# Performance work log

Measured on AMD Instinct MI355X. Metric: run time of the kernel, lower is better.

The kernel has to match this reference:

```python
import jax, jax.numpy as jnp
import numpy as np


def setup_inputs() -> dict:
    key = jax.random.key(0)
    kq, kk, kv = jax.random.split(key, 3)
    B, S, D = 4, 4096, 64
    q = jax.random.normal(kq, (B, S, D), dtype=jnp.float32)
    k = jax.random.normal(kk, (B, S, D), dtype=jnp.float32)
    v = jax.random.normal(kv, (B, S, D), dtype=jnp.float32)
    return {"q": q, "k": k, "v": v}


def reference(q, k, v):
    # Faithful math of the original blocked loop:
    #   output_i += exp(Q_i @ K_j^T) @ V_j, summed over all column blocks j
    # which is exactly unnormalized exponential attention:
    #   out = exp(Q K^T) V  (no 1/sqrt(d) scaling, no softmax normalization,
    #   no max-subtraction -- matching the source module's math).
    scores = jnp.einsum("bqd,bkd->bqk", q, k)  # [B, Sq, Sk]
    return jnp.einsum("bqk,bkd->bqd", jnp.exp(scores), v)  # [B, Sq, D]
```

## Files before the change

kernel.cpp:

```cpp
#include <hip/hip_runtime.h>
#include <hip/hip_bf16.h>


typedef short    s16x4 __attribute__((ext_vector_type(4)));
typedef short    s16x8 __attribute__((ext_vector_type(8)));
typedef _Float16 h16x8 __attribute__((ext_vector_type(8)));
typedef float    fx4   __attribute__((ext_vector_type(4)));
typedef float    fx16  __attribute__((ext_vector_type(16)));

constexpr int S = 4096, D = 64, BQ = 64, BN = 64;
constexpr int KH = 4;
constexpr int NT = S / BN / KH;

__device__ __forceinline__ unsigned short f2bf(float x) {
    unsigned u = __float_as_uint(x);
    u = (u + 0x7FFFu + ((u >> 16) & 1u)) >> 16;
    return (unsigned short)u;
}
__device__ __forceinline__ float bf2f(unsigned short h) {
    return __uint_as_float(((unsigned)h) << 16);
}
__device__ __forceinline__ unsigned short f2h(float x) {
    union { _Float16 h; unsigned short s; } u;
    u.h = (_Float16)x;
    return u.s;
}
__device__ __forceinline__ unsigned pack_bf16(float lo, float hi) {
    __hip_bfloat162 r = __float22bfloat162_rn(make_float2(lo, hi));
    union { __hip_bfloat162 b; unsigned u; } c;
    c.b = r;
    return c.u;
}

__global__ __launch_bounds__(256, 4) void attn_fused(
    const float* __restrict__ q, const float* __restrict__ k,
    const float* __restrict__ v, float* __restrict__ partial)
{
    __shared__ unsigned short Ks[64 * 72];
    __shared__ unsigned short Vt[64 * 72];
    __shared__ float red[4096];

    const int tid = threadIdx.x, lane = tid & 63, w = tid >> 6;
    const int h = lane >> 5, m5 = lane & 31;
    const int mt = w & 1, kkh = w >> 1;
    const int b = blockIdx.y, q0 = blockIdx.x * BQ, kh = blockIdx.z;

    const float* kbase = k + ((size_t)b * S + (size_t)kh * NT * BN) * D;
    const float* vbase = v + ((size_t)b * S + (size_t)kh * NT * BN) * D;

    h16x8 qf[4];
    {
        const float* qrow = q + ((size_t)b * S + q0 + mt * 32 + m5) * D + h * 8;
        #pragma unroll
        for (int ks = 0; ks < 4; ++ks) {
            float4 a = *(const float4*)(qrow + ks * 16);
            float4 c = *(const float4*)(qrow + ks * 16 + 4);
            qf[ks] = (h16x8){(_Float16)a.x, (_Float16)a.y, (_Float16)a.z, (_Float16)a.w,
                             (_Float16)c.x, (_Float16)c.y, (_Float16)c.z, (_Float16)c.w};
        }
    }

    const int krow0 = tid >> 4;
    const int kc4   = (tid & 15) << 2;
    const int vd    = tid & 63;
    const int vg    = w;

    float4 kraw[4];
    float  vraw[16];

    auto load_raw = [&](int t) {
        const float* kt = kbase + (size_t)t * BN * D;
        const float* vt = vbase + (size_t)t * BN * D;
        #pragma unroll
        for (int i = 0; i < 4; ++i)
            kraw[i] = *(const float4*)(kt + (i * 16 + krow0) * D + kc4);
        #pragma unroll
        for (int j = 0; j < 16; ++j)
            vraw[j] = vt[(vg * 16 + j) * D + vd];
    };

    auto cvt_store = [&]() {
        #pragma unroll
        for (int i = 0; i < 4; ++i) {
            s16x4 o = {(short)f2h(kraw[i].x), (short)f2h(kraw[i].y),
                       (short)f2h(kraw[i].z), (short)f2h(kraw[i].w)};
            *(s16x4*)&Ks[(i * 16 + krow0) * 72 + kc4] = o;
        }
        union { unsigned u[4]; s16x8 v; } p0, p1;
        #pragma unroll
        for (int jj = 0; jj < 4; ++jj) {
            p0.u[jj] = pack_bf16(vraw[2 * jj],     vraw[2 * jj + 1]);
            p1.u[jj] = pack_bf16(vraw[8 + 2 * jj], vraw[9 + 2 * jj]);
        }
        *(s16x8*)&Vt[vd * 72 + vg * 16]     = p0.v;
        *(s16x8*)&Vt[vd * 72 + vg * 16 + 8] = p1.v;
    };

    fx16 oacc[2] = {};

    load_raw(0);
    for (int t = 0; t < NT; ++t) {
        cvt_store();
        __syncthreads();
        if (t + 1 < NT) load_raw(t + 1);

        fx16 sa = {};
        #pragma unroll
        for (int ks = 0; ks < 4; ++ks) {
            h16x8 a = *(const h16x8*)&Ks[(kkh * 32 + m5) * 72 + ks * 16 + h * 8];
            sa = __builtin_amdgcn_mfma_f32_32x32x16_f16(a, qf[ks], sa, 0, 0, 0);
        }

        unsigned p01[8];
        #pragma unroll
        for (int rp = 0; rp < 8; ++rp)
            p01[rp] = pack_bf16(__expf(sa[2 * rp]), __expf(sa[2 * rp + 1]));

        union frag { unsigned u[4]; s16x8 v; };
        frag A[2];
#if __has_builtin(__builtin_amdgcn_permlane32_swap)
        typedef unsigned uix2 __attribute__((ext_vector_type(2)));
        uix2 r0 = __builtin_amdgcn_permlane32_swap(p01[0], p01[2], false, false);
        uix2 r1 = __builtin_amdgcn_permlane32_swap(p01[1], p01[3], false, false);
        A[0].u[0] = r0.x; A[0].u[1] = r1.x; A[0].u[2] = r0.y; A[0].u[3] = r1.y;
        uix2 r2 = __builtin_amdgcn_permlane32_swap(p01[4], p01[6], false, false);
        uix2 r3 = __builtin_amdgcn_permlane32_swap(p01[5], p01[7], false, false);
        A[1].u[0] = r2.x; A[1].u[1] = r3.x; A[1].u[2] = r2.y; A[1].u[3] = r3.y;
#else
        unsigned sw[8];
        #pragma unroll
        for (int rp = 0; rp < 8; ++rp)
            sw[rp] = (unsigned)__shfl_xor((int)p01[rp], 32, 64);
        A[0].u[0] = h ? sw[2]  : p01[0];
        A[0].u[1] = h ? sw[3]  : p01[1];
        A[0].u[2] = h ? p01[2] : sw[0];
        A[0].u[3] = h ? p01[3] : sw[1];
        A[1].u[0] = h ? sw[6]  : p01[4];
        A[1].u[1] = h ? sw[7]  : p01[5];
        A[1].u[2] = h ? p01[6] : sw[4];
        A[1].u[3] = h ? p01[7] : sw[5];
#endif

        #pragma unroll
        for (int ss = 0; ss < 2; ++ss)
            #pragma unroll
            for (int dt = 0; dt < 2; ++dt) {
                s16x8 vv = *(const s16x8*)&Vt[(dt * 32 + m5) * 72
                                              + kkh * 32 + ss * 16 + h * 8];
                oacc[dt] = __builtin_amdgcn_mfma_f32_32x32x16_bf16(
                    A[ss].v, vv, oacc[dt], 0, 0, 0);
            }

        __syncthreads();
    }

    if (kkh == 1) {
        #pragma unroll
        for (int dt = 0; dt < 2; ++dt)
            #pragma unroll
            for (int r = 0; r < 16; ++r)
                red[((mt * 2 + dt) * 16 + r) * 64 + lane] = oacc[dt][r];
    }
    __syncthreads();
    if (kkh == 0) {
        float* pout = partial + ((size_t)kh * 4 + b) * S * D;
        #pragma unroll
        for (int dt = 0; dt < 2; ++dt)
            #pragma unroll
            for (int r = 0; r < 16; ++r) {
                float val = oacc[dt][r] + red[((mt * 2 + dt) * 16 + r) * 64 + lane];
                int row = q0 + mt * 32 + (r & 3) + 8 * (r >> 2) + 4 * h;
                pout[(size_t)row * D + dt * 32 + m5] = val;
            }
    }
}

__global__ __launch_bounds__(256) void reduce4(
    const float4* __restrict__ p, float4* __restrict__ o, int n4, int stride4)
{
    int i = blockIdx.x * 256 + threadIdx.x;
    if (i < n4) {
        float4 a = p[i], b = p[i + stride4],
               c = p[i + 2 * stride4], d = p[i + 3 * stride4];
        o[i] = make_float4(a.x + b.x + c.x + d.x, a.y + b.y + c.y + d.y,
                           a.z + b.z + c.z + d.z, a.w + b.w + c.w + d.w);
    }
}

__global__ __launch_bounds__(1024) void attn_fallback(
    const float* __restrict__ q, const float* __restrict__ k,
    const float* __restrict__ v, float* __restrict__ out)
{
    __shared__ unsigned short Kh[64][72];
    __shared__ unsigned short Kl[64][72];
    __shared__ unsigned short Vs[64][68];
    __shared__ unsigned short Pf[64][72];

    const int tid = threadIdx.x, lane = tid & 63, wave = tid >> 6;
    const int quad = lane >> 4, tq = lane & 15;
    const int kkb = wave & 3, mba = wave >> 2;
    const int b = blockIdx.y, q0 = blockIdx.x * 64;
    const float* qb = q + (size_t)b * S * D;
    const float* kb = k + (size_t)b * S * D;
    const float* vb = v + (size_t)b * S * D;
    float* ob = out + (size_t)b * S * D;

    s16x8 qh[2], ql[2];
    {
        const float* qrow = qb + (size_t)(q0 + mba * 16 + tq) * D;
        #pragma unroll
        for (int ks = 0; ks < 2; ++ks) {
            const float* src = qrow + ks * 32 + quad * 8;
            float4 f0 = *(const float4*)src;
            float4 f1 = *(const float4*)(src + 4);
            float f[8] = {f0.x, f0.y, f0.z, f0.w, f1.x, f1.y, f1.z, f1.w};
            #pragma unroll
            for (int j = 0; j < 8; ++j) {
                unsigned short hh = f2bf(f[j]);
                qh[ks][j] = (short)hh;
                ql[ks][j] = (short)f2bf(f[j] - bf2f(hh));
            }
        }
    }
    fx4 oacc = {0.f, 0.f, 0.f, 0.f};
    const int krow = tid >> 4, kc4 = (tid & 15) << 2;
    const int vd = tid & 63, vk = (tid >> 6) << 2;

    for (int t = 0; t < S / 64; ++t) {
        __syncthreads();
        const float* kt = kb + (size_t)(t * 64 + krow) * D;
        const float* vt = vb + (size_t)(t * 64 + vk) * D;
        {
            float4 kv = *(const float4*)(kt + kc4);
            unsigned short h0 = f2bf(kv.x), h1 = f2bf(kv.y), h2 = f2bf(kv.z), h3 = f2bf(kv.w);
            s16x4 a = {(short)h0, (short)h1, (short)h2, (short)h3};
            s16x4 l4 = {(short)f2bf(kv.x - bf2f(h0)), (short)f2bf(kv.y - bf2f(h1)),
                        (short)f2bf(kv.z - bf2f(h2)), (short)f2bf(kv.w - bf2f(h3))};
            *(s16x4*)&Kh[krow][kc4] = a;
            *(s16x4*)&Kl[krow][kc4] = l4;
            const float* vs = vt + vd;
            s16x4 vv = {(short)f2bf(vs[0]), (short)f2bf(vs[D]),
                        (short)f2bf(vs[2 * D]), (short)f2bf(vs[3 * D])};
            *(s16x4*)&Vs[vd][vk] = vv;
        }
        __syncthreads();
        fx4 sacc = {0.f, 0.f, 0.f, 0.f};
        #pragma unroll
        for (int ks = 0; ks < 2; ++ks) {
            s16x8 kah = *(const s16x8*)&Kh[kkb * 16 + tq][ks * 32 + quad * 8];
            s16x8 kal = *(const s16x8*)&Kl[kkb * 16 + tq][ks * 32 + quad * 8];
            sacc = __builtin_amdgcn_mfma_f32_16x16x32_bf16(kah, qh[ks], sacc, 0, 0, 0);
            sacc = __builtin_amdgcn_mfma_f32_16x16x32_bf16(kah, ql[ks], sacc, 0, 0, 0);
            sacc = __builtin_amdgcn_mfma_f32_16x16x32_bf16(kal, qh[ks], sacc, 0, 0, 0);
        }
        s16x4 pp = {(short)f2bf(__expf(sacc[0])), (short)f2bf(__expf(sacc[1])),
                    (short)f2bf(__expf(sacc[2])), (short)f2bf(__expf(sacc[3]))};
        *(s16x4*)&Pf[mba * 16 + tq][kkb * 16 + (quad << 2)] = pp;
        __syncthreads();
        #pragma unroll
        for (int ks = 0; ks < 2; ++ks) {
            s16x8 pa = *(const s16x8*)&Pf[mba * 16 + tq][ks * 32 + quad * 8];
            const unsigned short* vr = &Vs[kkb * 16 + tq][ks * 32 + quad * 8];
            s16x4 va = *(const s16x4*)vr;
            s16x4 vb2 = *(const s16x4*)(vr + 4);
            s16x8 vfull = __builtin_shufflevector(va, vb2, 0, 1, 2, 3, 4, 5, 6, 7);
            oacc = __builtin_amdgcn_mfma_f32_16x16x32_bf16(pa, vfull, oacc, 0, 0, 0);
        }
    }
    #pragma unroll
    for (int r = 0; r < 4; ++r)
        ob[(size_t)(q0 + mba * 16 + quad * 4 + r) * D + kkb * 16 + tq] = oacc[r];
}

extern "C" void kernel_launch(void* const* d_in, const int* in_sizes, int n_in,
                              void* d_out, int out_size, void* d_ws, size_t ws_size,
                              hipStream_t stream) {
    const float* q = (const float*)d_in[0];
    const float* k = (const float*)d_in[1];
    const float* v = (const float*)d_in[2];
    float* out = (float*)d_out;
    const int nbatch = in_sizes[0] / (S * D);
    const size_t elems = (size_t)nbatch * S * D;

    const size_t need = (size_t)KH * elems * 4;
    if (nbatch == 4 && ws_size >= need && d_ws != nullptr) {
        float* partial = (float*)d_ws;
        dim3 grid(S / BQ, nbatch, KH);
        attn_fused<<<grid, 256, 0, stream>>>(q, k, v, partial);
        const int n4 = (int)(elems / 4);
        reduce4<<<(n4 + 255) / 256, 256, 0, stream>>>(
            (const float4*)partial, (float4*)out, n4, n4);
    } else {
        dim3 grid(S / 64, nbatch);
        attn_fallback<<<grid, 1024, 0, stream>>>(q, k, v, out);
    }
}
```

Baseline: 98.97 us.

## Double-buffer K/V tiles in LDS and use cheaper bf16 packing

Splits shared memory into two K/V buffers so the convert-and-store of the next tile and the global load two tiles ahead overlap with compute on the current tile, leaving one barrier per iteration instead of two. The reduction scratch now reuses the same LDS region. It also swaps the round-to-nearest-even bf16 pack for a cheaper add-and-permute pack, which rounds ties away from zero. LDS use goes from about 34KB to about 36KB, and more registers stay live.

```diff
diff --git a/kernel.cpp b/kernel.cpp
--- a/kernel.cpp
+++ b/kernel.cpp
@@ -11,6 +11,8 @@
 constexpr int S = 4096, D = 64, BQ = 64, BN = 64;
 constexpr int KH = 4;
 constexpr int NT = S / BN / KH;
+constexpr int KS_SH  = 64 * 72;
+constexpr int BUF_SH = 2 * KS_SH;
 
 __device__ __forceinline__ unsigned short f2bf(float x) {
     unsigned u = __float_as_uint(x);
@@ -25,20 +27,17 @@
     u.h = (_Float16)x;
     return u.s;
 }
-__device__ __forceinline__ unsigned pack_bf16(float lo, float hi) {
-    __hip_bfloat162 r = __float22bfloat162_rn(make_float2(lo, hi));
-    union { __hip_bfloat162 b; unsigned u; } c;
-    c.b = r;
-    return c.u;
-}
-
-__global__ __launch_bounds__(256, 4) void attn_fused(
+__device__ __forceinline__ unsigned packbf(float lo, float hi) {
+    unsigned a = __float_as_uint(lo) + 0x8000u;
+    unsigned b = __float_as_uint(hi) + 0x8000u;
+    return __builtin_amdgcn_perm(b, a, 0x07060302u);
+}
+
+__global__ __launch_bounds__(256, 4) void attn_fused2(
     const float* __restrict__ q, const float* __restrict__ k,
     const float* __restrict__ v, float* __restrict__ partial)
 {
-    __shared__ unsigned short Ks[64 * 72];
-    __shared__ unsigned short Vt[64 * 72];
-    __shared__ float red[4096];
+    __shared__ unsigned short smem[2 * BUF_SH];
 
     const int tid = threadIdx.x, lane = tid & 63, w = tid >> 6;
     const int h = lane >> 5, m5 = lane & 31;
@@ -79,42 +78,42 @@
             vraw[j] = vt[(vg * 16 + j) * D + vd];
     };
 
-    auto cvt_store = [&]() {
+    auto cvt_store = [&](int bi) {
+        unsigned short* Ksb = smem + bi * BUF_SH;
+        unsigned short* Vtb = Ksb + KS_SH;
         #pragma unroll
         for (int i = 0; i < 4; ++i) {
             s16x4 o = {(short)f2h(kraw[i].x), (short)f2h(kraw[i].y),
                        (short)f2h(kraw[i].z), (short)f2h(kraw[i].w)};
-            *(s16x4*)&Ks[(i * 16 + krow0) * 72 + kc4] = o;
+            *(s16x4*)&Ksb[(i * 16 + krow0) * 72 + kc4] = o;
         }
         union { unsigned u[4]; s16x8 v; } p0, p1;
         #pragma unroll
         for (int jj = 0; jj < 4; ++jj) {
-            p0.u[jj] = pack_bf16(vraw[2 * jj],     vraw[2 * jj + 1]);
-            p1.u[jj] = pack_bf16(vraw[8 + 2 * jj], vraw[9 + 2 * jj]);
-        }
-        *(s16x8*)&Vt[vd * 72 + vg * 16]     = p0.v;
-        *(s16x8*)&Vt[vd * 72 + vg * 16 + 8] = p1.v;
+            p0.u[jj] = packbf(vraw[2 * jj],     vraw[2 * jj + 1]);
+            p1.u[jj] = packbf(vraw[8 + 2 * jj], vraw[9 + 2 * jj]);
+        }
+        *(s16x8*)&Vtb[vd * 72 + vg * 16]     = p0.v;
+        *(s16x8*)&Vtb[vd * 72 + vg * 16 + 8] = p1.v;
     };
 
     fx16 oacc[2] = {};
 
-    load_raw(0);
-    for (int t = 0; t < NT; ++t) {
-        cvt_store();
-        __syncthreads();
-        if (t + 1 < NT) load_raw(t + 1);
+    auto compute = [&](int bi) {
+        const unsigned short* Ksb = smem + bi * BUF_SH;
+        const unsigned short* Vtb = Ksb + KS_SH;
 
         fx16 sa = {};
         #pragma unroll
         for (int ks = 0; ks < 4; ++ks) {
-            h16x8 a = *(const h16x8*)&Ks[(kkh * 32 + m5) * 72 + ks * 16 + h * 8];
+            h16x8 a = *(const h16x8*)&Ksb[(kkh * 32 + m5) * 72 + ks * 16 + h * 8];
             sa = __builtin_amdgcn_mfma_f32_32x32x16_f16(a, qf[ks], sa, 0, 0, 0);
         }
 
         unsigned p01[8];
         #pragma unroll
         for (int rp = 0; rp < 8; ++rp)
-            p01[rp] = pack_bf16(__expf(sa[2 * rp]), __expf(sa[2 * rp + 1]));
+            p01[rp] = packbf(__expf(sa[2 * rp]), __expf(sa[2 * rp + 1]));
 
         union frag { unsigned u[4]; s16x8 v; };
         frag A[2];
@@ -145,15 +144,25 @@
         for (int ss = 0; ss < 2; ++ss)
             #pragma unroll
             for (int dt = 0; dt < 2; ++dt) {
-                s16x8 vv = *(const s16x8*)&Vt[(dt * 32 + m5) * 72
-                                              + kkh * 32 + ss * 16 + h * 8];
+                s16x8 vv = *(const s16x8*)&Vtb[(dt * 32 + m5) * 72
+                                               + kkh * 32 + ss * 16 + h * 8];
                 oacc[dt] = __builtin_amdgcn_mfma_f32_32x32x16_bf16(
                     A[ss].v, vv, oacc[dt], 0, 0, 0);
             }
-
+    };
+
+    load_raw(0);
+    cvt_store(0);
+    load_raw(1);
+    for (int t = 0; t < NT; ++t) {
         __syncthreads();
-    }
-
+        if (t + 1 < NT) cvt_store((t + 1) & 1);
+        if (t + 2 < NT) load_raw(t + 2);
+        compute(t & 1);
+    }
+
+    __syncthreads();
+    float* red = (float*)smem;
     if (kkh == 1) {
         #pragma unroll
         for (int dt = 0; dt < 2; ++dt)
@@ -286,7 +295,7 @@
     if (nbatch == 4 && ws_size >= need && d_ws != nullptr) {
         float* partial = (float*)d_ws;
         dim3 grid(S / BQ, nbatch, KH);
-        attn_fused<<<grid, 256, 0, stream>>>(q, k, v, partial);
+        attn_fused2<<<grid, 256, 0, stream>>>(q, k, v, partial);
         const int n4 = (int)(elems / 4);
         reduce4<<<(n4 + 255) / 256, 256, 0, stream>>>(
             (const float4*)partial, (float4*)out, n4, n4);
```

Result: no change. 100.2 us (+1.3%).
